# Kernel optimization log

Hardware: AMD Instinct MI355X
Metric: run time of the kernel (lower is better)

## Reference

```python
import jax, jax.numpy as jnp
import numpy as np

N = 100000
E = 1600000
D_IN = 128
D_OUT = 128


def setup_inputs() -> dict:
    key = jax.random.key(0)
    k1, k2, k3, k4 = jax.random.split(key, 4)
    x = jax.random.normal(k1, (N, D_IN), dtype=jnp.float32)
    edge_index = jax.random.randint(k2, (2, E), 0, N, dtype=jnp.int64)
    # GCNConv params: glorot weight, zero bias
    scale = jnp.sqrt(6.0 / (D_IN + D_OUT)).astype(jnp.float32)
    W = jax.random.uniform(k3, (D_IN, D_OUT), dtype=jnp.float32, minval=-scale, maxval=scale)
    b = jnp.zeros((D_OUT,), dtype=jnp.float32)
    return {"x": x, "edge_index": edge_index, "W": W, "b": b}


def reference(x, edge_index, W, b):
    n = x.shape[0]
    # add self-loops (PyG GCNConv default: add_self_loops=True)
    loops = jnp.arange(n, dtype=edge_index.dtype)
    src = jnp.concatenate([edge_index[0], loops])
    dst = jnp.concatenate([edge_index[1], loops])
    # symmetric normalization: deg computed at target nodes
    ones = jnp.ones_like(dst, dtype=x.dtype)
    deg = jax.ops.segment_sum(ones, dst, num_segments=n)
    dinv = jnp.where(deg > 0, jax.lax.rsqrt(deg), 0.0)
    norm = dinv[src] * dinv[dst]  # [E+N]
    # linear transform then gather-scale-scatter aggregation
    h = x @ W  # [N, D_OUT]
    msgs = h[src] * norm[:, None]  # [E+N, D_OUT]
    out = jax.ops.segment_sum(msgs, dst, num_segments=n)
    return out + b
```

## Files before the change

### kernel.cpp

```cpp
#include <hip/hip_runtime.h>

#define D 128
#define CAP 5120

typedef __attribute__((ext_vector_type(4))) float f32x4;
typedef __attribute__((ext_vector_type(8))) short s16x8;

static __device__ __forceinline__ ushort f2bf(float f) {
    unsigned u = __float_as_uint(f);
    u += 0x7fffu + ((u >> 16) & 1u);
    return (ushort)(u >> 16);
}
static __device__ __forceinline__ float bf_lo(unsigned u) {
    return __uint_as_float(u << 16);
}
static __device__ __forceinline__ float bf_hi(unsigned u) {
    return __uint_as_float(u & 0xFFFF0000u);
}

__global__ __launch_bounds__(1024) void k_part(const int* __restrict__ src,
                                               const int* __restrict__ dst,
                                               int e, int nbins,
                                               int* __restrict__ gcursor,
                                               unsigned* __restrict__ praw) {
    __shared__ int hist[512];
    int tid = threadIdx.x;
    for (int j = tid; j < nbins; j += 1024) hist[j] = 0;
    __syncthreads();

    int chunk = (e + gridDim.x - 1) / gridDim.x;
    int lo = blockIdx.x * chunk;
    int hi = lo + chunk; if (hi > e) hi = e;

    for (int i = lo + tid; i < hi; i += 1024)
        atomicAdd(&hist[dst[i] >> 8], 1);
    __syncthreads();

    for (int j = tid; j < nbins; j += 1024)
        hist[j] = atomicAdd(&gcursor[j], hist[j]);
    __syncthreads();

    for (int i = lo + tid; i < hi; i += 1024) {
        int d = dst[i];
        int bin = d >> 8;
        int pos = atomicAdd(&hist[bin], 1);
        if (pos < CAP)
            praw[(size_t)bin * CAP + pos] = ((unsigned)(d & 255) << 24) | (unsigned)src[i];
    }
}

__global__ __launch_bounds__(1024) void k_fine(unsigned* __restrict__ praw,
                                               const int* __restrict__ gcursor,
                                               int n,
                                               int* __restrict__ deg,
                                               float* __restrict__ dinv,
                                               int* __restrict__ offs) {
    __shared__ int hist[256], scanv[256], cur[256];
    __shared__ unsigned stage[CAP];
    int b = blockIdx.x, tid = threadIdx.x;
    int base = b * CAP;
    int cnt = gcursor[b]; if (cnt > CAP) cnt = CAP;

    if (tid < 256) hist[tid] = 0;
    __syncthreads();
    for (int i = tid; i < cnt; i += 1024)
        atomicAdd(&hist[praw[base + i] >> 24], 1);
    __syncthreads();

    if (tid < 256) scanv[tid] = hist[tid];
    __syncthreads();
    for (int off = 1; off < 256; off <<= 1) {
        int t = 0;
        if (tid < 256 && tid >= off) t = scanv[tid - off];
        __syncthreads();
        if (tid < 256) scanv[tid] += t;
        __syncthreads();
    }
    if (tid < 256) {
        int ex = scanv[tid] - hist[tid];
        cur[tid] = ex;
        int d0 = b * 256 + tid;
        if (d0 < n) {
            deg[d0]  = hist[tid];
            dinv[d0] = rsqrtf((float)hist[tid] + 1.f);
            offs[d0] = base + ex;
        }
    }
    __syncthreads();

    for (int i = tid; i < cnt; i += 1024) {
        unsigned p = praw[base + i];
        int pos = atomicAdd(&cur[p >> 24], 1);
        stage[pos] = p & 0xFFFFFFu;
    }
    __syncthreads();
    for (int i = tid; i < cnt; i += 1024)
        praw[base + i] = stage[i];
}

__global__ __launch_bounds__(256) void k_wt(const float* __restrict__ W,
                                            ushort* __restrict__ WT) {
    int i = blockIdx.x * 256 + threadIdx.x;
    int nn = i >> 7, k = i & 127;
    WT[i] = f2bf(W[k * D + nn]);
}

__global__ __launch_bounds__(256, 2) void k_gemm_mfma(const float* __restrict__ x,
                                                      const ushort* __restrict__ WT,
                                                      const float* __restrict__ dinv,
                                                      ushort* __restrict__ h,
                                                      int n, int nchunks) {
    int lane = threadIdx.x & 63;
    int wid  = threadIdx.x >> 6;
    int lr = lane & 15;
    int lk = lane >> 4;

    s16x8 bfrag[8][4];
#pragma unroll
    for (int nt = 0; nt < 8; ++nt)
#pragma unroll
        for (int kk = 0; kk < 4; ++kk)
            bfrag[nt][kk] = *reinterpret_cast<const s16x8*>(
                WT + (nt * 16 + lr) * D + kk * 32 + lk * 8);

    int stride = gridDim.x * 4;
    for (int chunk = blockIdx.x * 4 + wid; chunk < nchunks; chunk += stride) {
        int r0 = chunk * 16;
        int ar = r0 + lr;
        if (ar > n - 1) ar = n - 1;

        s16x8 afrag[4];
#pragma unroll
        for (int kk = 0; kk < 4; ++kk) {
            const float4* p = reinterpret_cast<const float4*>(x) +
                              (size_t)ar * 32 + kk * 8 + lk * 2;
            float4 u = p[0];
            float4 v = p[1];
            s16x8 a;
            a[0] = (short)f2bf(u.x); a[1] = (short)f2bf(u.y);
            a[2] = (short)f2bf(u.z); a[3] = (short)f2bf(u.w);
            a[4] = (short)f2bf(v.x); a[5] = (short)f2bf(v.y);
            a[6] = (short)f2bf(v.z); a[7] = (short)f2bf(v.w);
            afrag[kk] = a;
        }

        f32x4 acc[8];
#pragma unroll
        for (int nt = 0; nt < 8; ++nt) acc[nt] = (f32x4){0.f, 0.f, 0.f, 0.f};

#pragma unroll
        for (int kk = 0; kk < 4; ++kk)
#pragma unroll
            for (int nt = 0; nt < 8; ++nt)
                acc[nt] = __builtin_amdgcn_mfma_f32_16x16x32_bf16(
                    afrag[kk], bfrag[nt][kk], acc[nt], 0, 0, 0);

#pragma unroll
        for (int i = 0; i < 4; ++i) {
            int row = r0 + lk * 4 + i;
            if (row < n) {
                float di = dinv[row];
#pragma unroll
                for (int nt = 0; nt < 8; ++nt)
                    h[(size_t)row * D + nt * 16 + lr] = f2bf(acc[nt][i] * di);
            }
        }
    }
}

__global__ __launch_bounds__(256) void k_gather(const unsigned* __restrict__ pairs,
                                                const int* __restrict__ offs,
                                                const int* __restrict__ deg,
                                                const float* __restrict__ dinv,
                                                const ushort* __restrict__ h,
                                                const float* __restrict__ b,
                                                float* __restrict__ out, int n) {
    int g = (blockIdx.x * 256 + threadIdx.x) >> 4;
    if (g >= n) return;
    int lane = threadIdx.x & 15;
    const uint4* h16 = reinterpret_cast<const uint4*>(h);

    float a0, a1, a2, a3, a4, a5, a6, a7;
    {
        uint4 v = h16[(size_t)g * 16 + lane];
        a0 = bf_lo(v.x); a1 = bf_hi(v.x);
        a2 = bf_lo(v.y); a3 = bf_hi(v.y);
        a4 = bf_lo(v.z); a5 = bf_hi(v.z);
        a6 = bf_lo(v.w); a7 = bf_hi(v.w);
    }

    int st  = offs[g];
    int cnt = deg[g];
    int k = 0;
    for (; k + 3 < cnt; k += 4) {
        int s0 = (int)pairs[st + k];
        int s1 = (int)pairs[st + k + 1];
        int s2 = (int)pairs[st + k + 2];
        int s3 = (int)pairs[st + k + 3];
        uint4 v0 = h16[(size_t)s0 * 16 + lane];
        uint4 v1 = h16[(size_t)s1 * 16 + lane];
        uint4 v2 = h16[(size_t)s2 * 16 + lane];
        uint4 v3 = h16[(size_t)s3 * 16 + lane];
        a0 += bf_lo(v0.x) + bf_lo(v1.x) + bf_lo(v2.x) + bf_lo(v3.x);
        a1 += bf_hi(v0.x) + bf_hi(v1.x) + bf_hi(v2.x) + bf_hi(v3.x);
        a2 += bf_lo(v0.y) + bf_lo(v1.y) + bf_lo(v2.y) + bf_lo(v3.y);
        a3 += bf_hi(v0.y) + bf_hi(v1.y) + bf_hi(v2.y) + bf_hi(v3.y);
        a4 += bf_lo(v0.z) + bf_lo(v1.z) + bf_lo(v2.z) + bf_lo(v3.z);
        a5 += bf_hi(v0.z) + bf_hi(v1.z) + bf_hi(v2.z) + bf_hi(v3.z);
        a6 += bf_lo(v0.w) + bf_lo(v1.w) + bf_lo(v2.w) + bf_lo(v3.w);
        a7 += bf_hi(v0.w) + bf_hi(v1.w) + bf_hi(v2.w) + bf_hi(v3.w);
    }
    for (; k < cnt; ++k) {
        int s0 = (int)pairs[st + k];
        uint4 v0 = h16[(size_t)s0 * 16 + lane];
        a0 += bf_lo(v0.x); a1 += bf_hi(v0.x);
        a2 += bf_lo(v0.y); a3 += bf_hi(v0.y);
        a4 += bf_lo(v0.z); a5 += bf_hi(v0.z);
        a6 += bf_lo(v0.w); a7 += bf_hi(v0.w);
    }

    float dd = dinv[g];
    const float4* b4 = reinterpret_cast<const float4*>(b);
    float4 blo = b4[lane * 2], bhi = b4[lane * 2 + 1];
    float4 olo, ohi;
    olo.x = a0 * dd + blo.x; olo.y = a1 * dd + blo.y;
    olo.z = a2 * dd + blo.z; olo.w = a3 * dd + blo.w;
    ohi.x = a4 * dd + bhi.x; ohi.y = a5 * dd + bhi.y;
    ohi.z = a6 * dd + bhi.z; ohi.w = a7 * dd + bhi.w;
    float4* o4 = reinterpret_cast<float4*>(out + (size_t)g * D + lane * 8);
    o4[0] = olo;
    o4[1] = ohi;
}

extern "C" void kernel_launch(void* const* d_in, const int* in_sizes, int n_in,
                              void* d_out, int out_size, void* d_ws, size_t ws_size,
                              hipStream_t stream) {
    const float* x  = (const float*)d_in[0];
    const int*   ei = (const int*)d_in[1];
    const float* W  = (const float*)d_in[2];
    const float* b  = (const float*)d_in[3];
    float* out = (float*)d_out;

    int n = in_sizes[0] / D;
    int e = in_sizes[1] / 2;
    const int* src = ei;
    const int* dst = ei + e;
    int nbins = (n + 255) >> 8;

    char* ws = (char*)d_ws;
    ushort*   h       = (ushort*)ws;    ws += (size_t)n * D * 2;
    ushort*   WT      = (ushort*)ws;    ws += (size_t)D * D * 2;
    int*      deg     = (int*)ws;       ws += (size_t)n * 4;
    float*    dinv    = (float*)ws;     ws += (size_t)n * 4;
    int*      offs    = (int*)ws;       ws += (size_t)n * 4;
    int*      gcursor = (int*)ws;       ws += 512 * 4;
    unsigned* praw    = (unsigned*)ws;

    hipMemsetAsync(gcursor, 0, 512 * 4, stream);

    k_part<<<256, 1024, 0, stream>>>(src, dst, e, nbins, gcursor, praw);

    k_fine<<<nbins, 1024, 0, stream>>>(praw, gcursor, n, deg, dinv, offs);

    k_wt<<<64, 256, 0, stream>>>(W, WT);

    int nchunks = (n + 15) / 16;
    k_gemm_mfma<<<512, 256, 0, stream>>>(x, WT, dinv, h, n, nchunks);

    int nb = (n * 16 + 255) / 256;
    k_gather<<<nb, 256, 0, stream>>>(praw, offs, deg, dinv, h, b, out, n);
}
```

Before: 121.3 us.

## Fold cursor zeroing into weight transpose, unroll gather by 8, halve partition grid

Removes the separate hipMemsetAsync by having the weight-transpose kernel zero the global bin cursors, and moves that kernel ahead of partitioning, so one fewer operation is launched. The gather loop now issues eight independent neighbour-row loads per iteration instead of four, to keep more memory requests in flight. The partition kernel grid is halved to 128 blocks, which gives each block more edges and fewer global cursor atomics but less parallelism. The summation order in the gather changes slightly, and the wider unroll raises register use.

```diff
diff --git a/kernel.cpp b/kernel.cpp
--- a/kernel.cpp
+++ b/kernel.cpp
@@ -16,6 +16,15 @@
 }
 static __device__ __forceinline__ float bf_hi(unsigned u) {
     return __uint_as_float(u & 0xFFFF0000u);
+}
+
+__global__ __launch_bounds__(256) void k_wt(const float* __restrict__ W,
+                                            ushort* __restrict__ WT,
+                                            int* __restrict__ gcursor) {
+    int i = blockIdx.x * 256 + threadIdx.x;
+    if (blockIdx.x < 2) gcursor[blockIdx.x * 256 + threadIdx.x] = 0;
+    int nn = i >> 7, k = i & 127;
+    WT[i] = f2bf(W[k * D + nn]);
 }
 
 __global__ __launch_bounds__(1024) void k_part(const int* __restrict__ src,
@@ -98,13 +107,6 @@
         praw[base + i] = stage[i];
 }
 
-__global__ __launch_bounds__(256) void k_wt(const float* __restrict__ W,
-                                            ushort* __restrict__ WT) {
-    int i = blockIdx.x * 256 + threadIdx.x;
-    int nn = i >> 7, k = i & 127;
-    WT[i] = f2bf(W[k * D + nn]);
-}
-
 __global__ __launch_bounds__(256, 2) void k_gemm_mfma(const float* __restrict__ x,
                                                       const ushort* __restrict__ WT,
                                                       const float* __restrict__ dinv,
@@ -192,23 +194,36 @@
     int st  = offs[g];
     int cnt = deg[g];
     int k = 0;
-    for (; k + 3 < cnt; k += 4) {
-        int s0 = (int)pairs[st + k];
-        int s1 = (int)pairs[st + k + 1];
-        int s2 = (int)pairs[st + k + 2];
-        int s3 = (int)pairs[st + k + 3];
-        uint4 v0 = h16[(size_t)s0 * 16 + lane];
-        uint4 v1 = h16[(size_t)s1 * 16 + lane];
-        uint4 v2 = h16[(size_t)s2 * 16 + lane];
-        uint4 v3 = h16[(size_t)s3 * 16 + lane];
-        a0 += bf_lo(v0.x) + bf_lo(v1.x) + bf_lo(v2.x) + bf_lo(v3.x);
-        a1 += bf_hi(v0.x) + bf_hi(v1.x) + bf_hi(v2.x) + bf_hi(v3.x);
-        a2 += bf_lo(v0.y) + bf_lo(v1.y) + bf_lo(v2.y) + bf_lo(v3.y);
-        a3 += bf_hi(v0.y) + bf_hi(v1.y) + bf_hi(v2.y) + bf_hi(v3.y);
-        a4 += bf_lo(v0.z) + bf_lo(v1.z) + bf_lo(v2.z) + bf_lo(v3.z);
-        a5 += bf_hi(v0.z) + bf_hi(v1.z) + bf_hi(v2.z) + bf_hi(v3.z);
-        a6 += bf_lo(v0.w) + bf_lo(v1.w) + bf_lo(v2.w) + bf_lo(v3.w);
-        a7 += bf_hi(v0.w) + bf_hi(v1.w) + bf_hi(v2.w) + bf_hi(v3.w);
+    for (; k + 7 < cnt; k += 8) {
+        uint4 v[8];
+#pragma unroll
+        for (int j = 0; j < 8; ++j) {
+            int s0 = (int)pairs[st + k + j];
+            v[j] = h16[(size_t)s0 * 16 + lane];
+        }
+#pragma unroll
+        for (int j = 0; j < 8; ++j) {
+            a0 += bf_lo(v[j].x); a1 += bf_hi(v[j].x);
+            a2 += bf_lo(v[j].y); a3 += bf_hi(v[j].y);
+            a4 += bf_lo(v[j].z); a5 += bf_hi(v[j].z);
+            a6 += bf_lo(v[j].w); a7 += bf_hi(v[j].w);
+        }
+    }
+    if (k + 3 < cnt) {
+        uint4 v[4];
+#pragma unroll
+        for (int j = 0; j < 4; ++j) {
+            int s0 = (int)pairs[st + k + j];
+            v[j] = h16[(size_t)s0 * 16 + lane];
+        }
+#pragma unroll
+        for (int j = 0; j < 4; ++j) {
+            a0 += bf_lo(v[j].x); a1 += bf_hi(v[j].x);
+            a2 += bf_lo(v[j].y); a3 += bf_hi(v[j].y);
+            a4 += bf_lo(v[j].z); a5 += bf_hi(v[j].z);
+            a6 += bf_lo(v[j].w); a7 += bf_hi(v[j].w);
+        }
+        k += 4;
     }
     for (; k < cnt; ++k) {
         int s0 = (int)pairs[st + k];
@@ -256,13 +271,11 @@
     int*      gcursor = (int*)ws;       ws += 512 * 4;
     unsigned* praw    = (unsigned*)ws;
 
-    hipMemsetAsync(gcursor, 0, 512 * 4, stream);
-
-    k_part<<<256, 1024, 0, stream>>>(src, dst, e, nbins, gcursor, praw);
+    k_wt<<<64, 256, 0, stream>>>(W, WT, gcursor);
+
+    k_part<<<128, 1024, 0, stream>>>(src, dst, e, nbins, gcursor, praw);
 
     k_fine<<<nbins, 1024, 0, stream>>>(praw, gcursor, n, deg, dinv, offs);
-
-    k_wt<<<64, 256, 0, stream>>>(W, WT);
 
     int nchunks = (n + 15) / 16;
     k_gemm_mfma<<<512, 256, 0, stream>>>(x, WT, dinv, h, n, nchunks);
```

After: 122.6 us. No clear change (+1.1%).
